# Optimization experiments

Measured on AMD Instinct MI355X. Metric: run time of the kernel, lower is better.

## Reference

```python
import jax, jax.numpy as jnp
import numpy as np

N_HEAD = 16


def setup_inputs() -> dict:
    key = jax.random.key(0)
    ks = jax.random.split(key, 6)
    B, T, C = 8, 1024, 1024
    s = 0.02
    return {
        "x": jax.random.normal(ks[0], (B, T, C), dtype=jnp.float32),
        "Wk": jax.random.normal(ks[1], (C, C), dtype=jnp.float32) * s,
        "bk": jnp.zeros((C,), dtype=jnp.float32),
        "Wq": jax.random.normal(ks[2], (C, C), dtype=jnp.float32) * s,
        "bq": jnp.zeros((C,), dtype=jnp.float32),
        "Wv": jax.random.normal(ks[3], (C, C), dtype=jnp.float32) * s,
        "bv": jnp.zeros((C,), dtype=jnp.float32),
        "Wp": jax.random.normal(ks[4], (C, C), dtype=jnp.float32) * s,
        "bp": jnp.zeros((C,), dtype=jnp.float32),
    }


def reference(x, Wk, bk, Wq, bq, Wv, bv, Wp, bp):
    B, T, C = x.shape
    H = N_HEAD
    d = C // H
    # QKV projections, split heads -> [B, H, T, d]
    k = (x @ Wk + bk).reshape(B, T, H, d).transpose(0, 2, 1, 3)
    q = (x @ Wq + bq).reshape(B, T, H, d).transpose(0, 2, 1, 3)
    v = (x @ Wv + bv).reshape(B, T, H, d).transpose(0, 2, 1, 3)
    # NOTE: original computes K @ Q^T (not Q @ K^T) and scales by C^-0.5
    attn = jnp.einsum('bhid,bhjd->bhij', k, q) * (C ** -0.5)
    mask = jnp.tril(jnp.ones((T, T), dtype=bool))  # tril==0 positions masked
    attn = jnp.where(mask, attn, -jnp.inf)
    attn = jax.nn.softmax(attn, axis=-1)
    out = jnp.einsum('bhij,bhjd->bhid', attn, v)  # [B, H, T, d]
    out = out.transpose(0, 2, 1, 3).reshape(B, T, C)
    return out @ Wp + bp
```

## Files before the change

kernel.cpp:

```cpp
#include <hip/hip_runtime.h>

typedef unsigned short u16;
typedef unsigned int u32;
typedef __bf16 bf16x8 __attribute__((ext_vector_type(8)));
typedef float f32x4 __attribute__((ext_vector_type(4)));

__device__ __forceinline__ u16 f2bf(float f) {
  u32 u = __builtin_bit_cast(u32, f);
  u += 0x7fffu + ((u >> 16) & 1u);
  return (u16)(u >> 16);
}

#define GLOAD_LDS16(g, l) __builtin_amdgcn_global_load_lds( \
    (const __attribute__((address_space(1))) void*)(g),     \
    (__attribute__((address_space(3))) void*)(l), 16, 0, 0)

#define SCK (0.03125f * 1.44269504088896f)

#define BARF() do { asm volatile("" ::: "memory"); \
                    __builtin_amdgcn_s_barrier();  \
                    asm volatile("" ::: "memory"); } while (0)

__global__ __launch_bounds__(256) void prep_k(const float* __restrict__ x,
                                              const float* __restrict__ W0,
                                              const float* __restrict__ W1,
                                              const float* __restrict__ W2,
                                              const float* __restrict__ W3,
                                              u16* __restrict__ xb,
                                              u16* __restrict__ WT) {
  __shared__ float tile[64][65];
  const int tid = threadIdx.x;
  if (blockIdx.x < 4096) {
    size_t i = (size_t)blockIdx.x * 256 + tid;
    const float4* p = reinterpret_cast<const float4*>(x) + i * 2;
    float4 a = p[0], b = p[1];
    u32 w0 = f2bf(a.x) | ((u32)f2bf(a.y) << 16);
    u32 w1 = f2bf(a.z) | ((u32)f2bf(a.w) << 16);
    u32 w2 = f2bf(b.x) | ((u32)f2bf(b.y) << 16);
    u32 w3 = f2bf(b.z) | ((u32)f2bf(b.w) << 16);
    uint4 o; o.x = w0; o.y = w1; o.z = w2; o.w = w3;
    *reinterpret_cast<uint4*>(xb + i * 8) = o;
    return;
  }
  const int bid2 = blockIdx.x - 4096;
  const int z = bid2 >> 8, kt = bid2 & 15, nt = (bid2 >> 4) & 15;
  const float* W = z == 0 ? W0 : z == 1 ? W1 : z == 2 ? W2 : W3;
  u16* dst = WT + (size_t)z * 1024 * 1024;
  const int k0 = kt * 64, n0 = nt * 64;
  const int rr = tid >> 4, c4 = (tid & 15) * 4;
#pragma unroll
  for (int p = 0; p < 4; ++p) {
    int r = rr + p * 16;
    float4 v = *reinterpret_cast<const float4*>(W + (size_t)(k0 + r) * 1024 + n0 + c4);
    tile[r][c4 + 0] = v.x; tile[r][c4 + 1] = v.y;
    tile[r][c4 + 2] = v.z; tile[r][c4 + 3] = v.w;
  }
  __syncthreads();
#pragma unroll
  for (int p = 0; p < 4; ++p) {
    int nl = rr + p * 16;
    u32 w0 = f2bf(tile[c4 + 0][nl]) | ((u32)f2bf(tile[c4 + 1][nl]) << 16);
    u32 w1 = f2bf(tile[c4 + 2][nl]) | ((u32)f2bf(tile[c4 + 3][nl]) << 16);
    uint2 o; o.x = w0; o.y = w1;
    *reinterpret_cast<uint2*>(dst + (size_t)(n0 + nl) * 1024 + k0 + c4) = o;
  }
}

template <int MODE>
__global__ __launch_bounds__(512, 2) void gemm8_k(
    const u16* __restrict__ A, const u16* __restrict__ BT,
    const float* __restrict__ bias0, const float* __restrict__ bias1,
    const float* __restrict__ bias2,
    u16* __restrict__ out_k, u16* __restrict__ out_q, u16* __restrict__ out_vT,
    float* __restrict__ out_f) {
  constexpr int BN = (MODE == 0) ? 192 : 128;
  constexpr int NB = BN / 64;
  constexpr int LPT = 4 + NB;
  constexpr int WCW = BN / 4;

  __shared__ __align__(16) u16 As[2][256 * 64];
  __shared__ __align__(16) u16 Bs[2][BN * 64];

  const int tid = threadIdx.x;
  const int w = tid >> 6, lane = tid & 63;
  const int wr = w >> 2, wc = w & 3;
  const int fr = lane & 15, fq = lane >> 4;
  const int d = fr & 7;

  const int bid = (int)blockIdx.x;
  const int xcd = bid & 7, c = bid >> 3;
  int bx, by;
  if constexpr (MODE == 0) {
    bx = (xcd & 3) * 8 + (c >> 3);
    by = (xcd >> 2) * 8 + (c & 7);
  } else {
    bx = xcd * 4 + (c >> 3);
    by = c & 7;
  }
  const int row0 = bx * 256, col0 = by * BN;

  const int r0 = tid >> 3;
  const int cbg = (tid & 7) ^ (r0 & 7);
  const u16* Asrc = A + (size_t)(row0 + r0) * 1024 + cbg * 8;
  const u16* Bsrc = BT + (size_t)(col0 + r0) * 1024 + cbg * 8;

#define STAGE8(buf, t) do {                                                  \
    _Pragma("unroll")                                                        \
    for (int sw = 0; sw < 4; ++sw)                                           \
      GLOAD_LDS16(Asrc + (size_t)sw * 65536 + (t) * 64,                      \
                  &As[buf][sw * 4096 + tid * 8]);                            \
    _Pragma("unroll")                                                        \
    for (int sw = 0; sw < NB; ++sw)                                          \
      GLOAD_LDS16(Bsrc + (size_t)sw * 65536 + (t) * 64,                      \
                  &Bs[buf][sw * 4096 + tid * 8]);                            \
  } while (0)

#define AOFF(mb, kk) ((wr * 128 + (mb) * 16 + fr) * 128 + (((((kk) << 2) | fq) ^ d) << 4))
#define BOFF(nb, kk) ((wc * WCW + (nb) * 16 + fr) * 128 + (((((kk) << 2) | fq) ^ d) << 4))

  f32x4 acc[8][NB] = {};

  STAGE8(0, 0);
  STAGE8(1, 1);
  asm volatile("s_waitcnt vmcnt(%0)" :: "n"(LPT) : "memory");
  BARF();

#pragma unroll 1
  for (int g = 0; g < 16; ++g) {
    const int buf = g & 1;
    const char* Ac = (const char*)&As[buf][0];
    const char* Bc = (const char*)&Bs[buf][0];
    bf16x8 a03[4][2], a47[4][2], b[NB][2];

#pragma unroll
    for (int mb = 0; mb < 4; ++mb) a03[mb][0] = *(const bf16x8*)(Ac + AOFF(mb, 0));
#pragma unroll
    for (int nb = 0; nb < NB; ++nb) b[nb][0] = *(const bf16x8*)(Bc + BOFF(nb, 0));
#pragma unroll
    for (int nb = 0; nb < NB; ++nb) b[nb][1] = *(const bf16x8*)(Bc + BOFF(nb, 1));
#pragma unroll
    for (int mb = 0; mb < 4; ++mb) a03[mb][1] = *(const bf16x8*)(Ac + AOFF(mb, 1));
    asm volatile("s_waitcnt lgkmcnt(%0)" :: "n"(NB + 4) : "memory");
    __builtin_amdgcn_s_setprio(1);
#pragma unroll
    for (int mb = 0; mb < 4; ++mb)
#pragma unroll
      for (int nb = 0; nb < NB; ++nb)
        acc[mb][nb] = __builtin_amdgcn_mfma_f32_16x16x32_bf16(
            a03[mb][0], b[nb][0], acc[mb][nb], 0, 0, 0);
    __builtin_amdgcn_s_setprio(0);
    BARF();

    asm volatile("s_waitcnt lgkmcnt(0)" ::: "memory");
    __builtin_amdgcn_s_setprio(1);
#pragma unroll
    for (int mb = 0; mb < 4; ++mb)
#pragma unroll
      for (int nb = 0; nb < NB; ++nb)
        acc[mb][nb] = __builtin_amdgcn_mfma_f32_16x16x32_bf16(
            a03[mb][1], b[nb][1], acc[mb][nb], 0, 0, 0);
    __builtin_amdgcn_s_setprio(0);
    BARF();

#pragma unroll
    for (int mb = 0; mb < 4; ++mb) a47[mb][0] = *(const bf16x8*)(Ac + AOFF(4 + mb, 0));
#pragma unroll
    for (int mb = 0; mb < 4; ++mb) a47[mb][1] = *(const bf16x8*)(Ac + AOFF(4 + mb, 1));
    asm volatile("s_waitcnt lgkmcnt(4)" ::: "memory");
    __builtin_amdgcn_s_setprio(1);
#pragma unroll
    for (int mb = 0; mb < 4; ++mb)
#pragma unroll
      for (int nb = 0; nb < NB; ++nb)
        acc[4 + mb][nb] = __builtin_amdgcn_mfma_f32_16x16x32_bf16(
            a47[mb][0], b[nb][0], acc[4 + mb][nb], 0, 0, 0);
    __builtin_amdgcn_s_setprio(0);
    asm volatile("s_waitcnt lgkmcnt(0)" ::: "memory");
    BARF();

    if (g + 2 < 16) STAGE8(buf, g + 2);
    __builtin_amdgcn_s_setprio(1);
#pragma unroll
    for (int mb = 0; mb < 4; ++mb)
#pragma unroll
      for (int nb = 0; nb < NB; ++nb)
        acc[4 + mb][nb] = __builtin_amdgcn_mfma_f32_16x16x32_bf16(
            a47[mb][1], b[nb][1], acc[4 + mb][nb], 0, 0, 0);
    __builtin_amdgcn_s_setprio(0);
    if (g <= 13)      asm volatile("s_waitcnt vmcnt(%0)" :: "n"(LPT) : "memory");
    else if (g == 14) asm volatile("s_waitcnt vmcnt(0)" ::: "memory");
    BARF();
  }
#undef STAGE8
#undef AOFF
#undef BOFF

  if constexpr (MODE == 0) {
#pragma unroll
    for (int mb = 0; mb < 8; ++mb) {
#pragma unroll
      for (int nb = 0; nb < NB; ++nb) {
        const int rg = row0 + wr * 128 + mb * 16 + fq * 4;
        const int cg = col0 + wc * WCW + nb * 16 + fr;
        const int which = cg >> 10;
        const int nloc = cg & 1023;
        const float bv = (which == 0 ? bias0 : which == 1 ? bias1 : bias2)[nloc];
        if (which == 0) {
#pragma unroll
          for (int r = 0; r < 4; ++r)
            out_k[(size_t)(rg + r) * 1024 + nloc] = f2bf((acc[mb][nb][r] + bv) * SCK);
        } else if (which == 1) {
#pragma unroll
          for (int r = 0; r < 4; ++r)
            out_q[(size_t)(rg + r) * 1024 + nloc] = f2bf(acc[mb][nb][r] + bv);
        } else {
          const int bb = rg >> 10, t = rg & 1023;
          const int hh = nloc >> 6, dl = nloc & 63;
          u32 w0 = f2bf(acc[mb][nb][0] + bv) | ((u32)f2bf(acc[mb][nb][1] + bv) << 16);
          u32 w1 = f2bf(acc[mb][nb][2] + bv) | ((u32)f2bf(acc[mb][nb][3] + bv) << 16);
          uint2 ov; ov.x = w0; ov.y = w1;
          *reinterpret_cast<uint2*>(out_vT + ((size_t)(bb * 16 + hh) * 64 + dl) * 1024 + t) = ov;
        }
      }
    }
  } else {
#pragma unroll
    for (int mb = 0; mb < 8; ++mb)
#pragma unroll
      for (int nb = 0; nb < NB; ++nb) {
        const int rg = row0 + wr * 128 + mb * 16 + fq * 4;
        const int cg = col0 + wc * WCW + nb * 16 + fr;
        const float bv = bias0[cg];
#pragma unroll
        for (int r = 0; r < 4; ++r)
          out_f[(size_t)(rg + r) * 1024 + cg] = acc[mb][nb][r] + bv;
      }
  }
}

__global__ __launch_bounds__(256, 4) void attn_k(const u16* __restrict__ Q,
                                                 const u16* __restrict__ K,
                                                 const u16* __restrict__ vT,
                                                 u16* __restrict__ O) {
  __shared__ __align__(16) u16 KsA[4096], KsB[4096], VsA[4096], VsB[4096];
  __shared__ __align__(16) u16 Plds[4][16][40];
  const int tid = threadIdx.x;
  const int w = tid >> 6, lane = tid & 63;
  const int fr = lane & 15, fq = lane >> 4, koff = fq * 8;

  const int n = blockIdx.x + 8 * (blockIdx.y + 16 * blockIdx.z);
  const int xcd = n & 7, rest = n >> 3;
  const int g = rest >> 3, pair = rest & 7;
  const int hb = xcd + 8 * g;
  const int h = hb & 15, b = hb >> 4;

  const size_t bstride = (size_t)1024 * 1024;
  const u16* Qb = Q + b * bstride + h * 64;
  const u16* Kg = K + b * bstride + h * 64;
  const u16* Vg = vT + ((size_t)(b * 16 + h) * 64) * 1024;

  const int srow = tid >> 3;
  const int scb = (tid & 7) ^ (srow & 7);
  const u16* KgT = Kg + (size_t)srow * 1024 + scb * 8;
  const u16* VgT = Vg + (size_t)srow * 1024 + scb * 8;

  const int vK0 = fr * 128 + ((fq ^ (fr & 7)) << 4);
  const int vK1 = vK0 ^ 64;
  const int pw = w * 1280 + fq * 320 + fr * 2;
  const int pr = w * 1280 + fr * 80 + fq * 16;

#define STAGE(KS, VS, jt) do {                                          \
    GLOAD_LDS16(KgT + (size_t)(jt) * 65536, &KS[tid * 8]);              \
    GLOAD_LDS16(KgT + (size_t)(jt) * 65536 + 32 * 1024, &KS[2048 + tid * 8]); \
    GLOAD_LDS16(VgT + (jt) * 64, &VS[tid * 8]);                         \
    GLOAD_LDS16(VgT + (jt) * 64 + 32 * 1024, &VS[2048 + tid * 8]);      \
  } while (0)

#pragma unroll 1
  for (int ph = 0; ph < 2; ++ph) {
    const int T = ph ? (15 - pair) : pair;
    const int i0 = T * 64;
    const int ibase = i0 + w * 16;

    bf16x8 aq0 = *reinterpret_cast<const bf16x8*>(&Qb[(size_t)(ibase + fr) * 1024 + koff]);
    bf16x8 aq1 = *reinterpret_cast<const bf16x8*>(&Qb[(size_t)(ibase + fr) * 1024 + koff + 32]);

    f32x4 o[4] = {};
    float lp[4] = {0.f, 0.f, 0.f, 0.f};

    auto compute = [&](const u16* KS, const u16* VS, bool diag) {
      const char* Kc = reinterpret_cast<const char*>(KS);
      const char* Vc = reinterpret_cast<const char*>(VS);
      f32x4 s[4];
#pragma unroll
      for (int jc = 0; jc < 4; ++jc) {
        bf16x8 bk0 = *reinterpret_cast<const bf16x8*>(Kc + vK0 + jc * 2048);
        bf16x8 bk1 = *reinterpret_cast<const bf16x8*>(Kc + vK1 + jc * 2048);
        f32x4 z = {};
        z = __builtin_amdgcn_mfma_f32_16x16x32_bf16(aq0, bk0, z, 0, 0, 0);
        s[jc] = __builtin_amdgcn_mfma_f32_16x16x32_bf16(aq1, bk1, z, 0, 0, 0);
      }
      bf16x8 bv0[4], bv1[4];
#pragma unroll
      for (int dn = 0; dn < 4; ++dn) {
        bv0[dn] = *reinterpret_cast<const bf16x8*>(Vc + vK0 + dn * 2048);
        bv1[dn] = *reinterpret_cast<const bf16x8*>(Vc + vK1 + dn * 2048);
      }
      float p[4][4];
      if (diag) {
#pragma unroll
        for (int r = 0; r < 4; ++r) {
          const int il = w * 16 + fq * 4 + r;
#pragma unroll
          for (int jc = 0; jc < 4; ++jc) {
            const int jl = jc * 16 + fr;
            p[jc][r] = (jl <= il) ? __builtin_amdgcn_exp2f(s[jc][r]) : 0.f;
          }
        }
      } else {
#pragma unroll
        for (int r = 0; r < 4; ++r)
#pragma unroll
          for (int jc = 0; jc < 4; ++jc)
            p[jc][r] = __builtin_amdgcn_exp2f(s[jc][r]);
      }
#pragma unroll
      for (int r = 0; r < 4; ++r)
        lp[r] += (p[0][r] + p[1][r]) + (p[2][r] + p[3][r]);
      char* Pc = reinterpret_cast<char*>(&Plds[0][0][0]);
#pragma unroll
      for (int jh = 0; jh < 2; ++jh) {
#pragma unroll
        for (int r = 0; r < 4; ++r)
#pragma unroll
          for (int j2 = 0; j2 < 2; ++j2)
            *reinterpret_cast<u16*>(Pc + pw + r * 80 + j2 * 32) = f2bf(p[jh * 2 + j2][r]);
        bf16x8 ap = *reinterpret_cast<const bf16x8*>(Pc + pr);
#pragma unroll
        for (int dn = 0; dn < 4; ++dn)
          o[dn] = __builtin_amdgcn_mfma_f32_16x16x32_bf16(ap, jh ? bv1[dn] : bv0[dn],
                                                          o[dn], 0, 0, 0);
      }
    };

    STAGE(KsA, VsA, 0);
    int t = 0;
    while (true) {
      {
        const bool more = t < T;
        if (more) STAGE(KsB, VsB, t + 1);
        if (more) { asm volatile("s_waitcnt vmcnt(4)" ::: "memory"); }
        else      { asm volatile("s_waitcnt vmcnt(0)" ::: "memory"); }
        __builtin_amdgcn_s_barrier();
        compute(KsA, VsA, t == T);
        __builtin_amdgcn_s_barrier();
        if (!more) break;
        ++t;
      }
      {
        const bool more = t < T;
        if (more) STAGE(KsA, VsA, t + 1);
        if (more) { asm volatile("s_waitcnt vmcnt(4)" ::: "memory"); }
        else      { asm volatile("s_waitcnt vmcnt(0)" ::: "memory"); }
        __builtin_amdgcn_s_barrier();
        compute(KsB, VsB, t == T);
        __builtin_amdgcn_s_barrier();
        if (!more) break;
        ++t;
      }
    }

#pragma unroll
    for (int x = 1; x < 16; x <<= 1)
#pragma unroll
      for (int r = 0; r < 4; ++r) lp[r] += __shfl_xor(lp[r], x);
#pragma unroll
    for (int r = 0; r < 4; ++r) {
      const float inv = 1.f / lp[r];
      const int ig = ibase + fq * 4 + r;
#pragma unroll
      for (int dn = 0; dn < 4; ++dn)
        O[((size_t)b * 1024 + ig) * 1024 + h * 64 + dn * 16 + fr] = f2bf(o[dn][r] * inv);
    }
  }
#undef STAGE
}

extern "C" void kernel_launch(void* const* d_in, const int* in_sizes, int n_in,
                              void* d_out, int out_size, void* d_ws, size_t ws_size,
                              hipStream_t stream) {
  const float* x  = (const float*)d_in[0];
  const float* Wk = (const float*)d_in[1];
  const float* bk = (const float*)d_in[2];
  const float* Wq = (const float*)d_in[3];
  const float* bq = (const float*)d_in[4];
  const float* Wv = (const float*)d_in[5];
  const float* bv = (const float*)d_in[6];
  const float* Wp = (const float*)d_in[7];
  const float* bp = (const float*)d_in[8];
  float* out = (float*)d_out;

  char* ws = (char*)d_ws;
  u16* xb   = (u16*)(ws);
  u16* WT   = (u16*)(ws + ((size_t)16 << 20));
  u16* kbuf = (u16*)(ws + ((size_t)24 << 20));
  u16* qbuf = (u16*)(ws + ((size_t)40 << 20));
  u16* vT   = (u16*)(ws + ((size_t)56 << 20));
  u16* aout = (u16*)(ws + ((size_t)72 << 20));

  prep_k<<<5120, 256, 0, stream>>>(x, Wk, Wq, Wv, Wp, xb, WT);
  gemm8_k<0><<<512, 512, 0, stream>>>(xb, WT, bk, bq, bv,
                                      kbuf, qbuf, vT, nullptr);
  attn_k<<<dim3(8, 16, 8), 256, 0, stream>>>(kbuf, qbuf, vT, aout);
  gemm8_k<1><<<256, 512, 0, stream>>>(aout, WT + (size_t)3 * 1024 * 1024,
                                      bp, nullptr, nullptr,
                                      nullptr, nullptr, nullptr, out);
}
```

Measured before the change: 139.9 us.

## Restructure GEMM main loop into two phases with all A fragments preloaded

The inner k-loop of the bf16 MFMA GEMM now loads all eight A fragments and both B k-slices into registers at the start, instead of splitting A into two halves across four phases. The loop drops from four barriers per iteration to two, and the next-tile global-to-LDS prefetch is issued earlier, after the first MFMA half. This cuts barrier overhead and leaves more MFMA work to cover the prefetch latency. The cost is extra VGPRs for the 16 A fragments, which could pressure occupancy at launch bounds (512,2).

```diff
diff --git a/kernel.cpp b/kernel.cpp
--- a/kernel.cpp
+++ b/kernel.cpp
@@ -77,6 +77,7 @@
   constexpr int NB = BN / 64;
   constexpr int LPT = 4 + NB;
   constexpr int WCW = BN / 4;
+  constexpr int HALF = 8 + NB;
 
   __shared__ __align__(16) u16 As[2][256 * 64];
   __shared__ __align__(16) u16 Bs[2][BN * 64];
@@ -130,63 +131,40 @@
     const int buf = g & 1;
     const char* Ac = (const char*)&As[buf][0];
     const char* Bc = (const char*)&Bs[buf][0];
-    bf16x8 a03[4][2], a47[4][2], b[NB][2];
-
-#pragma unroll
-    for (int mb = 0; mb < 4; ++mb) a03[mb][0] = *(const bf16x8*)(Ac + AOFF(mb, 0));
+    bf16x8 a[8][2], b[NB][2];
+
+#pragma unroll
+    for (int mb = 0; mb < 8; ++mb) a[mb][0] = *(const bf16x8*)(Ac + AOFF(mb, 0));
 #pragma unroll
     for (int nb = 0; nb < NB; ++nb) b[nb][0] = *(const bf16x8*)(Bc + BOFF(nb, 0));
 #pragma unroll
+    for (int mb = 0; mb < 8; ++mb) a[mb][1] = *(const bf16x8*)(Ac + AOFF(mb, 1));
+#pragma unroll
     for (int nb = 0; nb < NB; ++nb) b[nb][1] = *(const bf16x8*)(Bc + BOFF(nb, 1));
-#pragma unroll
-    for (int mb = 0; mb < 4; ++mb) a03[mb][1] = *(const bf16x8*)(Ac + AOFF(mb, 1));
-    asm volatile("s_waitcnt lgkmcnt(%0)" :: "n"(NB + 4) : "memory");
+
+    asm volatile("s_waitcnt lgkmcnt(%0)" :: "n"(HALF) : "memory");
     __builtin_amdgcn_s_setprio(1);
 #pragma unroll
-    for (int mb = 0; mb < 4; ++mb)
+    for (int mb = 0; mb < 8; ++mb)
 #pragma unroll
       for (int nb = 0; nb < NB; ++nb)
         acc[mb][nb] = __builtin_amdgcn_mfma_f32_16x16x32_bf16(
-            a03[mb][0], b[nb][0], acc[mb][nb], 0, 0, 0);
+            a[mb][0], b[nb][0], acc[mb][nb], 0, 0, 0);
     __builtin_amdgcn_s_setprio(0);
+
+    asm volatile("s_waitcnt lgkmcnt(0)" ::: "memory");
     BARF();
-
-    asm volatile("s_waitcnt lgkmcnt(0)" ::: "memory");
+    if (g + 2 < 16) STAGE8(buf, g + 2);
+
     __builtin_amdgcn_s_setprio(1);
 #pragma unroll
-    for (int mb = 0; mb < 4; ++mb)
+    for (int mb = 0; mb < 8; ++mb)
 #pragma unroll
       for (int nb = 0; nb < NB; ++nb)
         acc[mb][nb] = __builtin_amdgcn_mfma_f32_16x16x32_bf16(
-            a03[mb][1], b[nb][1], acc[mb][nb], 0, 0, 0);
+            a[mb][1], b[nb][1], acc[mb][nb], 0, 0, 0);
     __builtin_amdgcn_s_setprio(0);
-    BARF();
-
-#pragma unroll
-    for (int mb = 0; mb < 4; ++mb) a47[mb][0] = *(const bf16x8*)(Ac + AOFF(4 + mb, 0));
-#pragma unroll
-    for (int mb = 0; mb < 4; ++mb) a47[mb][1] = *(const bf16x8*)(Ac + AOFF(4 + mb, 1));
-    asm volatile("s_waitcnt lgkmcnt(4)" ::: "memory");
-    __builtin_amdgcn_s_setprio(1);
-#pragma unroll
-    for (int mb = 0; mb < 4; ++mb)
-#pragma unroll
-      for (int nb = 0; nb < NB; ++nb)
-        acc[4 + mb][nb] = __builtin_amdgcn_mfma_f32_16x16x32_bf16(
-            a47[mb][0], b[nb][0], acc[4 + mb][nb], 0, 0, 0);
-    __builtin_amdgcn_s_setprio(0);
-    asm volatile("s_waitcnt lgkmcnt(0)" ::: "memory");
-    BARF();
-
-    if (g + 2 < 16) STAGE8(buf, g + 2);
-    __builtin_amdgcn_s_setprio(1);
-#pragma unroll
-    for (int mb = 0; mb < 4; ++mb)
-#pragma unroll
-      for (int nb = 0; nb < NB; ++nb)
-        acc[4 + mb][nb] = __builtin_amdgcn_mfma_f32_16x16x32_bf16(
-            a47[mb][1], b[nb][1], acc[4 + mb][nb], 0, 0, 0);
-    __builtin_amdgcn_s_setprio(0);
+
     if (g <= 13)      asm volatile("s_waitcnt vmcnt(%0)" :: "n"(LPT) : "memory");
     else if (g == 14) asm volatile("s_waitcnt vmcnt(0)" ::: "memory");
     BARF();
```

Result: faster. 132.7 us (-5.1%).
